# Kernel optimization log

Measured on AMD Instinct MI355X. Metric: run time of the kernel, lower is better.

## Reference

```python
import jax, jax.numpy as jnp
import numpy as np

S, G, N, E = 4, 3, 20000, 320000   # seq_len, num_graphs, nodes, edges
DIN = HID = OUT = 64


def setup_inputs() -> dict:
    key = jax.random.key(0)
    ks = jax.random.split(key, 12)
    s = 0.1  # weight scale ~ Glorot-ish for d=64
    return {
        "x": jax.random.normal(ks[0], (S, G, N, DIN), jnp.float32),
        "edge_index": jax.random.randint(ks[1], (S, G, 2, E), 0, N, dtype=jnp.int32),
        "W1l": jax.random.normal(ks[2], (G, DIN, HID), jnp.float32) * s,
        "W1r": jax.random.normal(ks[3], (G, DIN, HID), jnp.float32) * s,
        "b1": jnp.zeros((G, HID), jnp.float32),
        "W2l": jax.random.normal(ks[4], (G, HID, OUT), jnp.float32) * s,
        "W2r": jax.random.normal(ks[5], (G, HID, OUT), jnp.float32) * s,
        "b2": jnp.zeros((G, OUT), jnp.float32),
        "Wih": jax.random.normal(ks[6], (4 * OUT, OUT), jnp.float32) * s,
        "Whh": jax.random.normal(ks[7], (4 * OUT, OUT), jnp.float32) * s,
        "bih": jnp.zeros((4 * OUT,), jnp.float32),
        "bhh": jnp.zeros((4 * OUT,), jnp.float32),
    }


def _sage(x, ei, Wl, Wr, b):
    # PyG SAGEConv(aggr='mean'): out = mean_{j->i}(x_j) @ Wl + x_i @ Wr + b
    src, dst = ei[0], ei[1]
    n = x.shape[0]
    msg = jax.ops.segment_sum(x[src], dst, num_segments=n)          # [N, d]
    cnt = jax.ops.segment_sum(jnp.ones((ei.shape[1], 1), x.dtype), dst, num_segments=n)
    mean = jnp.where(cnt > 0, msg / jnp.maximum(cnt, 1.0), 0.0)
    return mean @ Wl + x @ Wr + b


def _gnn(x, ei, Wl1, Wr1, bb1, Wl2, Wr2, bb2):
    h = jnp.tanh(_sage(x, ei, Wl1, Wr1, bb1))
    return jnp.tanh(_sage(h, ei, Wl2, Wr2, bb2))


def reference(x, edge_index, W1l, W1r, b1, W2l, W2r, b2, Wih, Whh, bih, bhh):
    # vmap over graphs (each graph has its own conv weights), then over timesteps
    per_graph = jax.vmap(_gnn, in_axes=(0, 0, 0, 0, 0, 0, 0, 0))
    per_seq = jax.vmap(per_graph, in_axes=(0, 0, None, None, None, None, None, None))
    h = per_seq(x, edge_index, W1l, W1r, b1, W2l, W2r, b2)          # [S, G, N, OUT]
    # torch: per timestep stack graphs [G,N,O] -> transpose -> [N,G,O]; cat over seq on dim0
    lstm_in = jnp.transpose(h, (0, 2, 1, 3)).reshape(S * N, G, OUT)  # [B, T=G, OUT]
    B = lstm_in.shape[0]

    def step(carry, xt):
        hp, cp = carry
        gates = xt @ Wih.T + hp @ Whh.T + bih + bhh                 # [B, 4*OUT]
        i, f, g, o = jnp.split(gates, 4, axis=-1)                   # torch gate order i,f,g,o
        c = jax.nn.sigmoid(f) * cp + jax.nn.sigmoid(i) * jnp.tanh(g)
        hn = jax.nn.sigmoid(o) * jnp.tanh(c)
        return (hn, c), None

    init = (jnp.zeros((B, OUT), x.dtype), jnp.zeros((B, OUT), x.dtype))
    (h_last, _), _ = jax.lax.scan(step, init, jnp.transpose(lstm_in, (1, 0, 2)))
    return h_last  # [S*N, OUT] == lstm_out[:, -1, :].squeeze()
```

## Files before the change

kernel.cpp:

```cpp
#include <hip/hip_runtime.h>
#include <math.h>

#define S 4
#define G 3
#define NN 20000
#define EE 320000
#define D 64
#define SG (S*G)

#define RGS 32
#define RNODES2 625
#define BCAP 14336
#define CHUNKA 100

#define LTILES 313
#define LTASKS (12*LTILES)
#define LQ (LTASKS/8)
#define LR (LTASKS%8)
#define NGRP   (NN/16)

static __device__ __forceinline__ float rcpf(float x){ return __builtin_amdgcn_rcpf(x); }
static __device__ __forceinline__ float sigmf(float x){ return rcpf(1.0f + __expf(-x)); }
static __device__ __forceinline__ float tanhf_fast(float x){
    float t = __expf(2.0f*x);
    return 1.0f - 2.0f*rcpf(t + 1.0f);
}

static __device__ __forceinline__ unsigned short f2bf(float f){
    union { float f; unsigned u; } v; v.f = f;
    unsigned r = v.u + 0x7FFF + ((v.u >> 16) & 1);
    return (unsigned short)(r >> 16);
}

typedef short bf16x8 __attribute__((ext_vector_type(8)));
typedef float f32x4  __attribute__((ext_vector_type(4)));


__global__ __launch_bounds__(256) void binA_kernel(const int* __restrict__ ei,
                                                   int* __restrict__ bcur,
                                                   int* __restrict__ bkt){
    __shared__ int wcnt[4*RGS];
    __shared__ int wb[4*RGS];
    int chunk = blockIdx.x, sg = blockIdx.y;
    int tid = threadIdx.x, w = tid >> 6;
    const int* srcp = ei + (size_t)(sg*2 + 0)*EE;
    const int* dstp = ei + (size_t)(sg*2 + 1)*EE;
    const int EPC = EE/CHUNKA;
    int start = chunk*EPC, end = start + EPC;

    for (int it = 0; it < (EPC + 1023)/1024; ++it){
        if (tid < 4*RGS) wcnt[tid] = 0;
        __syncthreads();
        int e = start + it*1024 + tid*4;
        bool valid = e < end;
        int d_[4], s_[4], r_[4], dl_[4], rk_[4];
        if (valid){
            int4 d4 = *(const int4*)&dstp[e];
            int4 s4 = *(const int4*)&srcp[e];
            d_[0]=d4.x; d_[1]=d4.y; d_[2]=d4.z; d_[3]=d4.w;
            s_[0]=s4.x; s_[1]=s4.y; s_[2]=s4.z; s_[3]=s4.w;
            #pragma unroll
            for (int j = 0; j < 4; ++j){
                int r = d_[j] / RNODES2;
                r_[j]  = r;
                dl_[j] = d_[j] - r*RNODES2;
                rk_[j] = atomicAdd(&wcnt[w*RGS + r], 1);
            }
        }
        __syncthreads();
        if (tid < RGS){
            int c0 = wcnt[0*RGS+tid], c1 = wcnt[1*RGS+tid];
            int c2 = wcnt[2*RGS+tid], c3 = wcnt[3*RGS+tid];
            int tot = c0+c1+c2+c3;
            int gb = 0;
            if (tot > 0) gb = atomicAdd(&bcur[sg*RGS + tid], tot);
            wb[0*RGS+tid] = gb;
            wb[1*RGS+tid] = gb + c0;
            wb[2*RGS+tid] = gb + c0 + c1;
            wb[3*RGS+tid] = gb + c0 + c1 + c2;
        }
        __syncthreads();
        if (valid){
            #pragma unroll
            for (int j = 0; j < 4; ++j){
                int pos = wb[w*RGS + r_[j]] + rk_[j];
                if (pos < BCAP)
                    bkt[(size_t)(sg*RGS + r_[j])*BCAP + pos] = (dl_[j] << 15) | s_[j];
            }
        }
    }
}


__global__ __launch_bounds__(256) void buildB_kernel(int* __restrict__ bkt,
                                                     const int* __restrict__ bcur,
                                                     int* __restrict__ off2,
                                                     int* __restrict__ deg2,
                                                     int* __restrict__ nid2,
                                                     int* __restrict__ offU){
    __shared__ int hist[RNODES2];
    __shared__ int pref[RNODES2];
    __shared__ int seg[BCAP];
    __shared__ int sums[256];
    __shared__ int dh[64];
    int sg = blockIdx.x / RGS, rg = blockIdx.x % RGS;
    int tid = threadIdx.x;
    int cnt = bcur[sg*RGS + rg];
    if (cnt > BCAP) cnt = BCAP;
    size_t base = (size_t)(sg*RGS + rg)*BCAP;
    int gnode = sg*NN + rg*RNODES2;

    for (int i = tid; i < RNODES2; i += 256) hist[i] = 0;
    if (tid < 64) dh[tid] = 0;
    __syncthreads();
    for (int j = tid; j < cnt; j += 256)
        atomicAdd(&hist[bkt[base + j] >> 15], 1);
    __syncthreads();

    int lo = tid*3, hi = min(lo+3, RNODES2);
    int s = 0;
    for (int i = lo; i < hi; ++i) s += (hist[i] + 3) & ~3;
    sums[tid] = s; __syncthreads();
    for (int ofs = 1; ofs < 256; ofs <<= 1){
        int v = (tid >= ofs) ? sums[tid-ofs] : 0;
        __syncthreads();
        sums[tid] += v;
        __syncthreads();
    }
    int run = sums[tid] - s;
    for (int i = lo; i < hi; ++i){
        pref[i] = run;
        offU[gnode + i] = (int)base + run;
        run += (hist[i] + 3) & ~3;
    }
    __syncthreads();

    for (int i = tid; i < RNODES2; i += 256)
        atomicAdd(&dh[min(hist[i], 63)], 1);
    __syncthreads();
    if (tid == 0){
        int r = 0;
        for (int k = 0; k < 64; ++k){ int c = dh[k]; dh[k] = r; r += c; }
    }
    __syncthreads();
    for (int i = tid; i < RNODES2; i += 256){
        int pos = atomicAdd(&dh[min(hist[i], 63)], 1);
        off2[gnode + pos] = offU[gnode + i];
        deg2[gnode + pos] = hist[i];
        nid2[gnode + pos] = rg*RNODES2 + i;
    }
    __syncthreads();

    for (int j = tid; j < cnt; j += 256){
        int p = bkt[base + j];
        int slot = atomicAdd(&pref[p >> 15], 1);
        if (slot < BCAP) seg[slot] = p & 0x7FFF;
    }
    __syncthreads();

    int padtot = min(sums[255], BCAP);
    for (int j = tid; j < padtot; j += 256) bkt[base + j] = seg[j];
}


__global__ __launch_bounds__(256) void convert_kernel(const float* __restrict__ x,
                                                      unsigned short* __restrict__ xb){
    int idx = blockIdx.x*256 + threadIdx.x;
    if (idx >= SG*NN*16) return;
    float4 v = ((const float4*)x)[idx];
    uint2 pk;
    pk.x = (unsigned)f2bf(v.x) | ((unsigned)f2bf(v.y) << 16);
    pk.y = (unsigned)f2bf(v.z) | ((unsigned)f2bf(v.w) << 16);
    ((uint2*)xb)[idx] = pk;
}


__global__ __launch_bounds__(256) void wprep2_kernel(const float* __restrict__ W1l,
                                                     const float* __restrict__ W1r,
                                                     const float* __restrict__ W2l,
                                                     const float* __restrict__ W2r,
                                                     const float* __restrict__ Wih,
                                                     const float* __restrict__ Whh,
                                                     const float* __restrict__ bih,
                                                     const float* __restrict__ bhh,
                                                     unsigned short* __restrict__ WL1,
                                                     unsigned short* __restrict__ WL2,
                                                     unsigned short* __restrict__ Wt,
                                                     float* __restrict__ bc){
    int idx = blockIdx.x*256 + threadIdx.x;
    if (idx < 24576){
        int g = idx >> 13, rem = idx & 8191, col = rem >> 7, k = rem & 127;
        float v = (k < 64) ? W1l[((size_t)g*64 + k)*64 + col]
                           : W1r[((size_t)g*64 + (k-64))*64 + col];
        WL1[idx] = f2bf(v);
    } else if (idx < 49152){
        int t = idx - 24576;
        int g = t >> 13, rem = t & 8191, col = rem >> 7, k = rem & 127;
        float v = (k < 64) ? W2l[((size_t)g*64 + k)*64 + col]
                           : W2r[((size_t)g*64 + (k-64))*64 + col];
        WL2[t] = f2bf(v);
    } else if (idx < 81920){
        int t = idx - 49152;
        int col = t >> 7, k = t & 127;
        float v = (k < 64) ? Wih[col*64 + k] : Whh[col*64 + (k - 64)];
        Wt[t] = f2bf(v);
    } else if (idx < 82176){
        int t = idx - 81920;
        bc[t] = bih[t] + bhh[t];
    }
}


#define WP 72
#define SWZ(e) ((((e) >> 1) ^ ((e) >> 4)) & 7)

__global__ __launch_bounds__(256,4) void layer_kernel(const unsigned short* __restrict__ xb,
                                                    const int* __restrict__ off2,
                                                    const int* __restrict__ deg2,
                                                    const int* __restrict__ nid2,
                                                    const int* __restrict__ csr,
                                                    const unsigned short* __restrict__ WL,
                                                    const float* __restrict__ bias,
                                                    unsigned short* __restrict__ outb){
    __shared__ unsigned short sStage[4][4096];
    int L = blockIdx.x;
    int xcd = L & 7;
    int task = ((xcd < LR) ? xcd*(LQ+1) : LR*(LQ+1) + (xcd-LR)*LQ) + (L >> 3);
    int sg = task / LTILES;
    int tsel = task - sg*LTILES;
    int tile = (LTILES-1) - tsel;
    int g = sg % G;
    int tid = threadIdx.x;
    int wave = tid >> 6, lane = tid & 63;
    int r = lane & 15, q = lane >> 4;
    const char* inbc = (const char*)(xb + (size_t)sg*NN*D);
    unsigned short* stg = &sStage[wave][0];

    int gid = tile*4 + wave;
    bool wv = (gid < NGRP);

    union { uint4 u; bf16x8 v; } biu;
    {
        unsigned v_ = 0x3F80u << ((r & 1) * 16);
        bool on = ((r >> 3) == (q & 1));
        int w_ = (r & 7) >> 1;
        biu.u.x = (on && w_ == 0) ? v_ : 0u;
        biu.u.y = (on && w_ == 1) ? v_ : 0u;
        biu.u.z = (on && w_ == 2) ? v_ : 0u;
        biu.u.w = (on && w_ == 3) ? v_ : 0u;
    }
    bf16x8 BI = biu.v;

    int idx = sg*NN + gid*16 + r;
    int node = 0, dg = 0, a = 0;
    if (wv){
        node = nid2[idx];
        a    = off2[idx];
        dg   = deg2[idx];
    }
    int mx = dg;
    mx = max(mx, __shfl_xor(mx, 1));
    mx = max(mx, __shfl_xor(mx, 2));
    mx = max(mx, __shfl_xor(mx, 4));
    mx = max(mx, __shfl_xor(mx, 8));

    unsigned zoff0 = (((unsigned)((SG - sg)*NN)) << 7);

    int aG  = __shfl(a,  lane >> 2);
    int dgG = __shfl(dg, lane >> 2);

    f32x4 acc[4];
    #pragma unroll
    for (int cb = 0; cb < 4; ++cb) acc[cb] = (f32x4){0.f,0.f,0.f,0.f};

    int nch = (mx + 3) >> 2;
    for (int c = 0; c < nch; ++c){
        int sL = c*4 + (lane & 3);
        int nL = csr[aG + sL];
        unsigned adr = (sL < dgG) ? (((unsigned)nL) << 7) : zoff0;
        uint4 v[8];
        #pragma unroll
        for (int j = 0; j < 8; ++j){
            unsigned ae = (unsigned)__shfl((int)adr, j*8 + (lane >> 3));
            v[j] = *(const uint4*)(inbc + ae + (unsigned)((lane & 7) << 4));
        }
        #pragma unroll
        for (int j = 0; j < 8; ++j){
            int e = j*8 + (lane >> 3);
            int gr = ((lane & 7) ^ SWZ(e)) << 4;
            *(uint4*)((char*)stg + e*128 + gr) = v[j];
        }
        #pragma unroll
        for (int m = 0; m < 2; ++m){
            int e = r*4 + m*2 + (q >> 1);
            int ebase = e*128;
            int sw = SWZ(e) << 4;
            #pragma unroll
            for (int cb = 0; cb < 4; ++cb){
                int b = cb*32 + ((q & 1) << 4);
                bf16x8 af = *(const bf16x8*)((const char*)stg + ebase + (b ^ sw));
                acc[cb] = __builtin_amdgcn_mfma_f32_16x16x32_bf16(af, BI, acc[cb], 0, 0, 0);
            }
        }
    }

    asm volatile("" ::: "memory");
    unsigned short* sMw = stg;
    float inv[4];
    #pragma unroll
    for (int reg = 0; reg < 4; ++reg){
        int d = __shfl(dg, (q << 2) | reg, 16);
        inv[reg] = (d > 0) ? rcpf((float)d) : 0.0f;
    }
    #pragma unroll
    for (int cb = 0; cb < 4; ++cb)
        #pragma unroll
        for (int reg = 0; reg < 4; ++reg)
            sMw[(q*4 + reg)*WP + cb*16 + r] = f2bf(acc[cb][reg] * inv[reg]);
    asm volatile("" ::: "memory");

    const unsigned short* WLg = WL + (size_t)g*64*128;
    f32x4 accv[4];
    #pragma unroll
    for (int ct = 0; ct < 4; ++ct) accv[ct] = (f32x4){0.f,0.f,0.f,0.f};
    #pragma unroll
    for (int kc = 0; kc < 4; ++kc){
        bf16x8 af;
        if (kc < 2) af = *(const bf16x8*)&sMw[r*WP + kc*32 + q*8];
        else        af = *(const bf16x8*)(inbc + (((unsigned)node) << 7) + (unsigned)((kc-2)*64 + q*16));
        #pragma unroll
        for (int ct = 0; ct < 4; ++ct){
            bf16x8 bfr = *(const bf16x8*)&WLg[(ct*16 + r)*128 + kc*32 + q*8];
            accv[ct] = __builtin_amdgcn_mfma_f32_16x16x32_bf16(af, bfr, accv[ct], 0, 0, 0);
        }
    }

    asm volatile("" ::: "memory");
    unsigned short* sOw = stg + 2048;
    #pragma unroll
    for (int ct = 0; ct < 4; ++ct){
        float bv = bias[g*64 + ct*16 + r];
        #pragma unroll
        for (int reg = 0; reg < 4; ++reg)
            sOw[(q*4+reg)*WP + ct*16 + r] = f2bf(tanhf_fast(accv[ct][reg] + bv));
    }
    asm volatile("" ::: "memory");
    if (wv){
        #pragma unroll
        for (int pass = 0; pass < 2; ++pass){
            int rloc = pass*8 + (lane >> 3), chunk = lane & 7;
            int i2 = gid*16 + rloc;
            int nd = nid2[sg*NN + i2];
            uint4 v = *(const uint4*)&sOw[rloc*WP + chunk*8];
            *(uint4*)&outb[((size_t)sg*NN + nd)*D + chunk*8] = v;
        }
    }
}


__global__ __launch_bounds__(256) void lstm_kernel(const unsigned short* __restrict__ h2b,
                                                   const unsigned short* __restrict__ Wt,
                                                   const float* __restrict__ bc,
                                                   float* __restrict__ out){
    __shared__ unsigned short sH[64*WP];
    int tid = threadIdx.x;
    int b0 = blockIdx.x * 64;
    int wave = tid >> 6, lane = tid & 63;
    int n0 = lane & 15, q = lane >> 4;
    int jcol = wave*16 + n0;

    float bb[4];
    #pragma unroll
    for (int T = 0; T < 4; ++T) bb[T] = bc[T*64 + jcol];

    float c[4][4];
    #pragma unroll
    for (int rt = 0; rt < 4; ++rt)
        #pragma unroll
        for (int reg = 0; reg < 4; ++reg) c[rt][reg] = 0.0f;

    int s_[4], n_[4];
    #pragma unroll
    for (int rt = 0; rt < 4; ++rt){
        int b = b0 + rt*16 + n0;
        s_[rt] = b / NN; n_[rt] = b - s_[rt]*NN;
    }

    #pragma unroll
    for (int t = 0; t < G; ++t){
        f32x4 accv[4][4];
        #pragma unroll
        for (int rt = 0; rt < 4; ++rt)
            #pragma unroll
            for (int T = 0; T < 4; ++T) accv[rt][T] = (f32x4){0.f,0.f,0.f,0.f};

        int nkc = (t == 0) ? 2 : 4;
        #pragma unroll
        for (int kc = 0; kc < 4; ++kc){
            if (kc >= nkc) break;
            bf16x8 af[4];
            #pragma unroll
            for (int rt = 0; rt < 4; ++rt){
                if (kc < 2) af[rt] = *(const bf16x8*)&h2b[((size_t)(s_[rt]*G + t)*NN + n_[rt])*D + kc*32 + q*8];
                else        af[rt] = *(const bf16x8*)&sH[(rt*16 + n0)*WP + (kc-2)*32 + q*8];
            }
            #pragma unroll
            for (int T = 0; T < 4; ++T){
                int ct = T*4 + wave;
                bf16x8 bfr = *(const bf16x8*)&Wt[(ct*16 + n0)*128 + kc*32 + q*8];
                #pragma unroll
                for (int rt = 0; rt < 4; ++rt)
                    accv[rt][T] = __builtin_amdgcn_mfma_f32_16x16x32_bf16(af[rt], bfr, accv[rt][T], 0, 0, 0);
            }
        }
        if (t > 0) __syncthreads();

        #pragma unroll
        for (int rt = 0; rt < 4; ++rt){
            #pragma unroll
            for (int reg = 0; reg < 4; ++reg){
                float ig = sigmf(accv[rt][0][reg] + bb[0]);
                float fg = sigmf(accv[rt][1][reg] + bb[1]);
                float gg = tanhf_fast(accv[rt][2][reg] + bb[2]);
                float og = sigmf(accv[rt][3][reg] + bb[3]);
                float cn = fg*c[rt][reg] + ig*gg;
                c[rt][reg] = cn;
                float hv = og * tanhf_fast(cn);
                int row = rt*16 + q*4 + reg;
                if (t < G-1) sH[row*WP + jcol] = f2bf(hv);
                else         out[(size_t)(b0 + row)*D + jcol] = hv;
            }
        }
        if (t < G-1) __syncthreads();
    }
}


extern "C" void kernel_launch(void* const* d_in, const int* in_sizes, int n_in,
                              void* d_out, int out_size, void* d_ws, size_t ws_size,
                              hipStream_t stream) {
    const float* x   = (const float*)d_in[0];
    const int*   ei  = (const int*)  d_in[1];
    const float* W1l = (const float*)d_in[2];
    const float* W1r = (const float*)d_in[3];
    const float* b1  = (const float*)d_in[4];
    const float* W2l = (const float*)d_in[5];
    const float* W2r = (const float*)d_in[6];
    const float* b2  = (const float*)d_in[7];
    const float* Wih = (const float*)d_in[8];
    const float* Whh = (const float*)d_in[9];
    const float* bih = (const float*)d_in[10];
    const float* bhh = (const float*)d_in[11];
    float* out = (float*)d_out;

    char* ws = (char*)d_ws;
    size_t cur = 0;
    auto alloc = [&](size_t bytes)->void*{
        cur = (cur + 255) & ~(size_t)255;
        void* p = ws + cur; cur += bytes; return p;
    };
    int*   bkt  = (int*)alloc((size_t)SG*RGS*BCAP*4);
    int*   bcur = (int*)alloc((size_t)SG*RGS*4);
    int*   off2 = (int*)alloc((size_t)SG*NN*4);
    int*   deg2 = (int*)alloc((size_t)SG*NN*4);
    int*   nid2 = (int*)alloc((size_t)SG*NN*4);
    int*   offU = (int*)alloc((size_t)SG*NN*4);
    unsigned short* xb  = (unsigned short*)alloc(((size_t)SG*NN + 1)*D*2);
    unsigned short* h1b = (unsigned short*)alloc(((size_t)SG*NN + 1)*D*2);
    unsigned short* h2b = (unsigned short*)alloc((size_t)SG*NN*D*2);
    unsigned short* WL1 = (unsigned short*)alloc((size_t)G*64*128*2);
    unsigned short* WL2 = (unsigned short*)alloc((size_t)G*64*128*2);
    unsigned short* Wt  = (unsigned short*)alloc((size_t)256*128*2);
    float* bc   = (float*)alloc((size_t)256*4);
    (void)ws_size; (void)in_sizes; (void)n_in; (void)out_size;

    (void)hipMemsetAsync(bcur, 0, (size_t)SG*RGS*4, stream);
    (void)hipMemsetAsync(xb  + (size_t)SG*NN*D, 0, (size_t)D*2, stream);
    (void)hipMemsetAsync(h1b + (size_t)SG*NN*D, 0, (size_t)D*2, stream);

    convert_kernel<<<(SG*NN*16 + 255)/256, 256, 0, stream>>>(x, xb);
    binA_kernel  <<<dim3(CHUNKA, SG), 256, 0, stream>>>(ei, bcur, bkt);
    buildB_kernel<<<SG*RGS, 256, 0, stream>>>(bkt, bcur, off2, deg2, nid2, offU);
    wprep2_kernel<<<321, 256, 0, stream>>>(W1l, W1r, W2l, W2r, Wih, Whh, bih, bhh,
                                           WL1, WL2, Wt, bc);

    layer_kernel<<<LTASKS, 256, 0, stream>>>(xb,  off2, deg2, nid2, bkt, WL1, b1, h1b);
    layer_kernel<<<LTASKS, 256, 0, stream>>>(h1b, off2, deg2, nid2, bkt, WL2, b2, h2b);

    lstm_kernel <<<(S*NN)/64, 256, 0, stream>>>(h2b, Wt, bc, out);
}
```

Measured before the change: 382.3 us.

## Use one-wave blocks with double-buffered neighbor gathers in SAGE layer kernel

The layer kernel now runs one 64-thread wave per block, each handling a 16-node group, instead of four waves per 256-thread block. The neighbor-aggregation loop takes 2 neighbors per node per step instead of 4 and software-pipelines the work. CSR indices and gathered rows for upcoming chunks are loaded into two register buffers while the current chunk is staged to LDS and reduced with MFMA. The aim is to hide gather latency, cut padding waste for low-degree nodes, and skip nodes with no neighbors, at the cost of more blocks and smaller LDS stages.

```diff
diff --git a/kernel.cpp b/kernel.cpp
--- a/kernel.cpp
+++ b/kernel.cpp
@@ -13,11 +13,10 @@
 #define BCAP 14336
 #define CHUNKA 100
 
-#define LTILES 313
-#define LTASKS (12*LTILES)
-#define LQ (LTASKS/8)
-#define LR (LTASKS%8)
 #define NGRP   (NN/16)
+#define LT2    15024
+#define LT2PX  1878
+#define GPAD   1252
 
 static __device__ __forceinline__ float rcpf(float x){ return __builtin_amdgcn_rcpf(x); }
 static __device__ __forceinline__ float sigmf(float x){ return rcpf(1.0f + __expf(-x)); }
@@ -214,30 +213,56 @@
 #define WP 72
 #define SWZ(e) ((((e) >> 1) ^ ((e) >> 4)) & 7)
 
-__global__ __launch_bounds__(256,4) void layer_kernel(const unsigned short* __restrict__ xb,
-                                                    const int* __restrict__ off2,
-                                                    const int* __restrict__ deg2,
-                                                    const int* __restrict__ nid2,
-                                                    const int* __restrict__ csr,
-                                                    const unsigned short* __restrict__ WL,
-                                                    const float* __restrict__ bias,
-                                                    unsigned short* __restrict__ outb){
-    __shared__ unsigned short sStage[4][4096];
+#define LDIX(IX, CC) { IX = csr[aG2 + (CC)*2 + (lane & 1)]; }
+
+#define GATH(V, IX, CC) { \
+    int sL_ = (CC)*2 + (lane & 1); \
+    unsigned adr_ = (sL_ < dgG2) ? (((unsigned)(IX)) << 7) : zoff0; \
+    _Pragma("unroll") \
+    for (int j_ = 0; j_ < 4; ++j_){ \
+        unsigned ae_ = (unsigned)__shfl((int)adr_, j_*8 + (lane >> 3)); \
+        V[j_] = *(const uint4*)(inbc + ae_ + (unsigned)((lane & 7) << 4)); \
+    } \
+}
+
+#define CONSUME(V) { \
+    _Pragma("unroll") \
+    for (int j_ = 0; j_ < 4; ++j_){ \
+        int e_ = j_*8 + (lane >> 3); \
+        int gr_ = ((lane & 7) ^ SWZ(e_)) << 4; \
+        *(uint4*)((char*)stg + e_*128 + gr_) = V[j_]; \
+    } \
+    { \
+        int e_ = r*2 + (q >> 1); \
+        int eb_ = e_*128, sw_ = SWZ(e_) << 4; \
+        _Pragma("unroll") \
+        for (int cb_ = 0; cb_ < 4; ++cb_){ \
+            int b_ = cb_*32 + ((q & 1) << 4); \
+            bf16x8 af_ = *(const bf16x8*)((const char*)stg + eb_ + (b_ ^ sw_)); \
+            acc[cb_] = __builtin_amdgcn_mfma_f32_16x16x32_bf16(af_, BI, acc[cb_], 0, 0, 0); \
+        } \
+    } \
+}
+
+__global__ __launch_bounds__(64) void layer_kernel(const unsigned short* __restrict__ xb,
+                                                   const int* __restrict__ off2,
+                                                   const int* __restrict__ deg2,
+                                                   const int* __restrict__ nid2,
+                                                   const int* __restrict__ csr,
+                                                   const unsigned short* __restrict__ WL,
+                                                   const float* __restrict__ bias,
+                                                   unsigned short* __restrict__ outb){
+    __shared__ unsigned short stg[2048];
     int L = blockIdx.x;
-    int xcd = L & 7;
-    int task = ((xcd < LR) ? xcd*(LQ+1) : LR*(LQ+1) + (xcd-LR)*LQ) + (L >> 3);
-    int sg = task / LTILES;
-    int tsel = task - sg*LTILES;
-    int tile = (LTILES-1) - tsel;
+    int task = (L & 7)*LT2PX + (L >> 3);
+    int sg = task / GPAD;
+    int g0 = task - sg*GPAD;
+    int gid = (GPAD - 1) - g0;
+    if (gid >= NGRP) return;
     int g = sg % G;
-    int tid = threadIdx.x;
-    int wave = tid >> 6, lane = tid & 63;
+    int lane = threadIdx.x;
     int r = lane & 15, q = lane >> 4;
     const char* inbc = (const char*)(xb + (size_t)sg*NN*D);
-    unsigned short* stg = &sStage[wave][0];
-
-    int gid = tile*4 + wave;
-    bool wv = (gid < NGRP);
 
     union { uint4 u; bf16x8 v; } biu;
     {
@@ -252,12 +277,9 @@
     bf16x8 BI = biu.v;
 
     int idx = sg*NN + gid*16 + r;
-    int node = 0, dg = 0, a = 0;
-    if (wv){
-        node = nid2[idx];
-        a    = off2[idx];
-        dg   = deg2[idx];
-    }
+    int node = nid2[idx];
+    int a    = off2[idx];
+    int dg   = deg2[idx];
     int mx = dg;
     mx = max(mx, __shfl_xor(mx, 1));
     mx = max(mx, __shfl_xor(mx, 2));
@@ -266,40 +288,29 @@
 
     unsigned zoff0 = (((unsigned)((SG - sg)*NN)) << 7);
 
-    int aG  = __shfl(a,  lane >> 2);
-    int dgG = __shfl(dg, lane >> 2);
+    int aG2  = __shfl(a,  lane >> 1);
+    int dgG2 = __shfl(dg, lane >> 1);
 
     f32x4 acc[4];
     #pragma unroll
     for (int cb = 0; cb < 4; ++cb) acc[cb] = (f32x4){0.f,0.f,0.f,0.f};
 
-    int nch = (mx + 3) >> 2;
-    for (int c = 0; c < nch; ++c){
-        int sL = c*4 + (lane & 3);
-        int nL = csr[aG + sL];
-        unsigned adr = (sL < dgG) ? (((unsigned)nL) << 7) : zoff0;
-        uint4 v[8];
-        #pragma unroll
-        for (int j = 0; j < 8; ++j){
-            unsigned ae = (unsigned)__shfl((int)adr, j*8 + (lane >> 3));
-            v[j] = *(const uint4*)(inbc + ae + (unsigned)((lane & 7) << 4));
-        }
-        #pragma unroll
-        for (int j = 0; j < 8; ++j){
-            int e = j*8 + (lane >> 3);
-            int gr = ((lane & 7) ^ SWZ(e)) << 4;
-            *(uint4*)((char*)stg + e*128 + gr) = v[j];
-        }
-        #pragma unroll
-        for (int m = 0; m < 2; ++m){
-            int e = r*4 + m*2 + (q >> 1);
-            int ebase = e*128;
-            int sw = SWZ(e) << 4;
-            #pragma unroll
-            for (int cb = 0; cb < 4; ++cb){
-                int b = cb*32 + ((q & 1) << 4);
-                bf16x8 af = *(const bf16x8*)((const char*)stg + ebase + (b ^ sw));
-                acc[cb] = __builtin_amdgcn_mfma_f32_16x16x32_bf16(af, BI, acc[cb], 0, 0, 0);
+    if (mx > 0){
+        int nch = (mx + 1) >> 1;
+        uint4 vA[4], vB[4];
+        int ixA, ixB;
+        LDIX(ixA, 0);
+        LDIX(ixB, 1);
+        GATH(vA, ixA, 0);
+        if (nch > 1) GATH(vB, ixB, 1);
+        LDIX(ixA, 2);
+        LDIX(ixB, 3);
+        for (int c = 0; c < nch; c += 2){
+            CONSUME(vA);
+            if (c + 2 < nch){ GATH(vA, ixA, c + 2); LDIX(ixA, c + 4); }
+            if (c + 1 < nch){
+                CONSUME(vB);
+                if (c + 3 < nch){ GATH(vB, ixB, c + 3); LDIX(ixB, c + 5); }
             }
         }
     }
@@ -336,7 +347,7 @@
     }
 
     asm volatile("" ::: "memory");
-    unsigned short* sOw = stg + 2048;
+    unsigned short* sOw = stg;
     #pragma unroll
     for (int ct = 0; ct < 4; ++ct){
         float bv = bias[g*64 + ct*16 + r];
@@ -345,15 +356,13 @@
             sOw[(q*4+reg)*WP + ct*16 + r] = f2bf(tanhf_fast(accv[ct][reg] + bv));
     }
     asm volatile("" ::: "memory");
-    if (wv){
-        #pragma unroll
-        for (int pass = 0; pass < 2; ++pass){
-            int rloc = pass*8 + (lane >> 3), chunk = lane & 7;
-            int i2 = gid*16 + rloc;
-            int nd = nid2[sg*NN + i2];
-            uint4 v = *(const uint4*)&sOw[rloc*WP + chunk*8];
-            *(uint4*)&outb[((size_t)sg*NN + nd)*D + chunk*8] = v;
-        }
+    #pragma unroll
+    for (int pass = 0; pass < 2; ++pass){
+        int rloc = pass*8 + (lane >> 3), chunk = lane & 7;
+        int i2 = gid*16 + rloc;
+        int nd = nid2[sg*NN + i2];
+        uint4 v = *(const uint4*)&sOw[rloc*WP + chunk*8];
+        *(uint4*)&outb[((size_t)sg*NN + nd)*D + chunk*8] = v;
     }
 }
 
@@ -484,8 +493,8 @@
     wprep2_kernel<<<321, 256, 0, stream>>>(W1l, W1r, W2l, W2r, Wih, Whh, bih, bhh,
                                            WL1, WL2, Wt, bc);
 
-    layer_kernel<<<LTASKS, 256, 0, stream>>>(xb,  off2, deg2, nid2, bkt, WL1, b1, h1b);
-    layer_kernel<<<LTASKS, 256, 0, stream>>>(h1b, off2, deg2, nid2, bkt, WL2, b2, h2b);
+    layer_kernel<<<LT2, 64, 0, stream>>>(xb,  off2, deg2, nid2, bkt, WL1, b1, h1b);
+    layer_kernel<<<LT2, 64, 0, stream>>>(h1b, off2, deg2, nid2, bkt, WL2, b2, h2b);
 
     lstm_kernel <<<(S*NN)/64, 256, 0, stream>>>(h2b, Wt, bc, out);
 }
```

After: 602.6 us. 57.6% more time.
